# Kernel tuning notes

Hardware: AMD Instinct MI355X
Metric: run time of the kernel (lower is better)

The kernel has to match this reference:

```python
import jax, jax.numpy as jnp
import numpy as np

B, S, I, H = 256, 128, 1024, 512
SENT, DOC = 256, 512
SEGMENTS, MAX_POS = 4, 25
POS_SZ, SEG_SZ = 50, 50


def setup_inputs() -> dict:
    key = jax.random.key(0)
    ks = jax.random.split(key, 24)
    sc = 0.05
    rn = lambda k, shp: jax.random.normal(k, shp, jnp.float32) * sc
    pos_emb = rn(ks[20], (MAX_POS + 1, POS_SZ)).at[0].set(0.0)  # padding_idx=0
    seg_emb = rn(ks[22], (SEGMENTS + 1, SEG_SZ)).at[0].set(0.0)  # padding_idx=0
    return {
        "sentence_embeddings": jax.random.normal(ks[0], (B, S, I), jnp.float32),
        "num_sentences": jnp.full((B,), S, jnp.int32),
        "W_ih_f": rn(ks[1], (3 * H, I)), "W_hh_f": rn(ks[2], (3 * H, H)),
        "b_ih_f": jnp.zeros((3 * H,), jnp.float32), "b_hh_f": jnp.zeros((3 * H,), jnp.float32),
        "W_ih_b": rn(ks[3], (3 * H, I)), "W_hh_b": rn(ks[4], (3 * H, H)),
        "b_ih_b": jnp.zeros((3 * H,), jnp.float32), "b_hh_b": jnp.zeros((3 * H,), jnp.float32),
        "W_sent": rn(ks[5], (SENT, 2 * H)), "b_sent": jnp.zeros((SENT,), jnp.float32),
        "W_content": rn(ks[6], (1, SENT)), "b_content": jnp.zeros((1,), jnp.float32),
        "W_doc1": rn(ks[7], (DOC, SENT)), "b_doc1": jnp.zeros((DOC,), jnp.float32),
        "W_doc2": rn(ks[8], (SENT, DOC)), "b_doc2": jnp.zeros((SENT,), jnp.float32),
        "W_sim": rn(ks[9], (SENT, SENT)),
        "bias": jnp.zeros((1,), jnp.float32),
        "pos_emb": pos_emb, "W_pos": rn(ks[21], (1, POS_SZ)),
        "seg_emb": seg_emb, "W_seg": rn(ks[23], (1, SEG_SZ)),
    }


def _gru_dir(x_sbi, W_ih, W_hh, b_ih, b_hh):
    # x_sbi: [S,B,I] -> hidden states [S,B,H], PyTorch GRU gate order (r,z,n)
    h_dim = W_hh.shape[1]
    xp = jnp.einsum('sbi,gi->sbg', x_sbi, W_ih) + b_ih  # [S,B,3H]

    def step(h, xpt):
        gh = h @ W_hh.T + b_hh
        xr, xz, xn = jnp.split(xpt, 3, axis=-1)
        hr, hz, hn = jnp.split(gh, 3, axis=-1)
        r = jax.nn.sigmoid(xr + hr)
        z = jax.nn.sigmoid(xz + hz)
        n = jnp.tanh(xn + r * hn)
        h_new = (1.0 - z) * n + z * h
        return h_new, h_new

    h0 = jnp.zeros((x_sbi.shape[1], h_dim), x_sbi.dtype)
    _, hs = jax.lax.scan(step, h0, xp)
    return hs


def reference(sentence_embeddings, num_sentences, W_ih_f, W_hh_f, b_ih_f, b_hh_f,
              W_ih_b, W_hh_b, b_ih_b, b_hh_b, W_sent, b_sent, W_content, b_content,
              W_doc1, b_doc1, W_doc2, b_doc2, W_sim, bias, pos_emb, W_pos, seg_emb, W_seg):
    b, s, _ = sentence_embeddings.shape
    xt = jnp.swapaxes(sentence_embeddings, 0, 1)  # [S,B,I]
    fwd = _gru_dir(xt, W_ih_f, W_hh_f, b_ih_f, b_hh_f)
    bwd = _gru_dir(xt[::-1], W_ih_b, W_hh_b, b_ih_b, b_hh_b)[::-1]
    rnn_out = jnp.swapaxes(jnp.concatenate([fwd, bwd], -1), 0, 1)  # [B,S,2H]

    sent = jax.nn.relu(rnn_out @ W_sent.T + b_sent)              # [B,S,SENT]
    content = (sent @ W_content.T + b_content)[..., 0]            # [B,S]
    avg = sent.sum(1) / num_sentences[:, None].astype(sent.dtype) # [B,SENT]
    doc = jnp.tanh(avg @ W_doc1.T + b_doc1) @ W_doc2.T + b_doc2   # [B,SENT]
    salience = jnp.einsum('bsd,bd->bs', sent, doc)

    abs_pos = jnp.arange(1, s + 1)
    chunk = jnp.round(num_sentences.astype(jnp.float32) / SEGMENTS)[:, None]
    rel_pos = jnp.clip(jnp.ceil(abs_pos[None, :].astype(jnp.float32) / chunk), 0, SEGMENTS).astype(jnp.int32)
    abs_pos_c = jnp.clip(abs_pos, 0, MAX_POS)
    pos_logits = (pos_emb[abs_pos_c] @ W_pos.T)[..., 0][None, :]  # [1,S]
    seg_logits = (seg_emb[rel_pos] @ W_seg.T)[..., 0]             # [B,S]

    static = content + salience + pos_logits + seg_logits + bias  # [B,S]

    sent_t = jnp.swapaxes(sent, 0, 1)   # [S,B,SENT]
    static_t = static.T                  # [S,B]

    def step(summary, inp):
        s_t, st_t = inp
        nov = -jnp.einsum('bi,ij,bj->b', s_t, W_sim, jnp.tanh(summary))
        logit = st_t + nov
        summary = summary + s_t * jax.nn.sigmoid(logit)[:, None]
        return summary, logit

    _, logits_t = jax.lax.scan(step, jnp.zeros_like(sent_t[0]), (sent_t, static_t))
    return logits_t.T  # [B,S]
```

## Files before the change

kernel.cpp:

```cpp
#include <hip/hip_runtime.h>
#include <math.h>

#define B_    256
#define S_    128
#define I_    1024
#define H_    512
#define G3_   1536
#define SENT_ 256
#define DOC_  512
#define CH_   16

__device__ __forceinline__ float sigmoidf_(float x) { return 1.f / (1.f + expf(-x)); }

__global__ __launch_bounds__(256) void xp_gemm_kernel(
    const float* __restrict__ x,
    const float* __restrict__ Wf, const float* __restrict__ Wb,
    const float* __restrict__ bf, const float* __restrict__ bb,
    float* __restrict__ xq, int c0)
{
    const int nt   = blockIdx.x % 12;
    const int rest = blockIdx.x / 12;
    const int dir  = rest >> 5;
    const int mt   = rest & 31;
    const int m0   = mt * 128;
    const int n0   = nt * 128;
    const int tl   = m0 >> 8;
    const int b0x  = m0 & 255;
    const int s    = dir ? (S_ - 1 - (c0 + tl)) : (c0 + tl);
    const float* __restrict__ W    = dir ? Wb : Wf;
    const float* __restrict__ bias = dir ? bb : bf;
    float* __restrict__ outp = xq + (size_t)(dir * CH_ + tl) * B_ * G3_;

    __shared__ float Al[16][132];
    __shared__ float Bl[16][132];

    const int tid = threadIdx.x;
    const int tx = tid & 15, ty = tid >> 4;
    float acc[8][8] = {};

    for (int k0 = 0; k0 < I_; k0 += 16) {
        #pragma unroll
        for (int u = 0; u < 2; ++u) {
            const int fi = u * 256 + tid;
            const int r = fi >> 2, k4 = (fi & 3) * 4;
            const float4 v = *(const float4*)
                &x[((size_t)(b0x + r) * S_ + s) * (size_t)I_ + k0 + k4];
            Al[k4+0][r] = v.x; Al[k4+1][r] = v.y; Al[k4+2][r] = v.z; Al[k4+3][r] = v.w;
        }
        #pragma unroll
        for (int u = 0; u < 2; ++u) {
            const int fi = u * 256 + tid;
            const int c = fi >> 2, k4 = (fi & 3) * 4;
            const float4 v = *(const float4*)&W[(size_t)(n0 + c) * I_ + k0 + k4];
            Bl[k4+0][c] = v.x; Bl[k4+1][c] = v.y; Bl[k4+2][c] = v.z; Bl[k4+3][c] = v.w;
        }
        __syncthreads();
        #pragma unroll
        for (int k = 0; k < 16; ++k) {
            const float4 a0 = *(const float4*)&Al[k][ty * 4];
            const float4 a1 = *(const float4*)&Al[k][64 + ty * 4];
            const float4 b0 = *(const float4*)&Bl[k][tx * 4];
            const float4 b1 = *(const float4*)&Bl[k][64 + tx * 4];
            const float av[8] = {a0.x,a0.y,a0.z,a0.w,a1.x,a1.y,a1.z,a1.w};
            const float bv[8] = {b0.x,b0.y,b0.z,b0.w,b1.x,b1.y,b1.z,b1.w};
            #pragma unroll
            for (int i = 0; i < 8; ++i)
                #pragma unroll
                for (int jj = 0; jj < 8; ++jj)
                    acc[i][jj] += av[i] * bv[jj];
        }
        __syncthreads();
    }

    #pragma unroll
    for (int i = 0; i < 8; ++i) {
        const int rloc = (i < 4) ? (ty * 4 + i) : (64 + ty * 4 + (i - 4));
        const int b = b0x + rloc;
        #pragma unroll
        for (int cgv = 0; cgv < 2; ++cgv) {
            const int n = n0 + cgv * 64 + tx * 4;
            const float4 o = { acc[i][cgv*4+0] + bias[n+0],
                               acc[i][cgv*4+1] + bias[n+1],
                               acc[i][cgv*4+2] + bias[n+2],
                               acc[i][cgv*4+3] + bias[n+3] };
            *(float4*)&outp[(size_t)b * G3_ + n] = o;
        }
    }
}

__global__ __launch_bounds__(256) void sent_gemm_kernel(
    const float* __restrict__ A, const float* __restrict__ W,
    const float* __restrict__ bias, float* __restrict__ outp)
{
    const int nt = blockIdx.x & 1;
    const int mt = blockIdx.x >> 1;
    const int m0 = mt * 128, n0 = nt * 128;
    constexpr int K = 1024;

    __shared__ float Al[16][132];
    __shared__ float Bl[16][132];
    const int tid = threadIdx.x;
    const int tx = tid & 15, ty = tid >> 4;
    float acc[8][8] = {};

    for (int k0 = 0; k0 < K; k0 += 16) {
        #pragma unroll
        for (int u = 0; u < 2; ++u) {
            const int fi = u * 256 + tid;
            const int r = fi >> 2, k4 = (fi & 3) * 4;
            const float4 v = *(const float4*)&A[(size_t)(m0 + r) * K + k0 + k4];
            Al[k4+0][r] = v.x; Al[k4+1][r] = v.y; Al[k4+2][r] = v.z; Al[k4+3][r] = v.w;
        }
        #pragma unroll
        for (int u = 0; u < 2; ++u) {
            const int fi = u * 256 + tid;
            const int c = fi >> 2, k4 = (fi & 3) * 4;
            const float4 v = *(const float4*)&W[(size_t)(n0 + c) * K + k0 + k4];
            Bl[k4+0][c] = v.x; Bl[k4+1][c] = v.y; Bl[k4+2][c] = v.z; Bl[k4+3][c] = v.w;
        }
        __syncthreads();
        #pragma unroll
        for (int k = 0; k < 16; ++k) {
            const float4 a0 = *(const float4*)&Al[k][ty * 4];
            const float4 a1 = *(const float4*)&Al[k][64 + ty * 4];
            const float4 b0 = *(const float4*)&Bl[k][tx * 4];
            const float4 b1 = *(const float4*)&Bl[k][64 + tx * 4];
            const float av[8] = {a0.x,a0.y,a0.z,a0.w,a1.x,a1.y,a1.z,a1.w};
            const float bv[8] = {b0.x,b0.y,b0.z,b0.w,b1.x,b1.y,b1.z,b1.w};
            #pragma unroll
            for (int i = 0; i < 8; ++i)
                #pragma unroll
                for (int jj = 0; jj < 8; ++jj)
                    acc[i][jj] += av[i] * bv[jj];
        }
        __syncthreads();
    }

    #pragma unroll
    for (int i = 0; i < 8; ++i) {
        const int m = m0 + ((i < 4) ? (ty * 4 + i) : (64 + ty * 4 + (i - 4)));
        #pragma unroll
        for (int cgv = 0; cgv < 2; ++cgv) {
            const int n = n0 + cgv * 64 + tx * 4;
            const float4 o = { fmaxf(acc[i][cgv*4+0] + bias[n+0], 0.f),
                               fmaxf(acc[i][cgv*4+1] + bias[n+1], 0.f),
                               fmaxf(acc[i][cgv*4+2] + bias[n+2], 0.f),
                               fmaxf(acc[i][cgv*4+3] + bias[n+3], 0.f) };
            *(float4*)&outp[(size_t)m * SENT_ + n] = o;
        }
    }
}

__global__ __launch_bounds__(256) void gru_step_kernel(
    const float* __restrict__ xq,
    const float* __restrict__ Whf, const float* __restrict__ Whb,
    const float* __restrict__ bhf, const float* __restrict__ bhb,
    float* __restrict__ rnn, int t)
{
    __shared__ float hl[32][68];
    __shared__ float wl[3][32][66];

    const int bid = blockIdx.x;
    const int r8 = bid & 7;
    const int dir = (r8 < 4) ? 0 : 1;
    const int idx = (bid >> 3) * 4 + (r8 & 3);
    const int b0 = (idx >> 4) * 32;
    const int j0 = (idx & 15) * 32;
    const float* __restrict__ Wh = dir ? Whb : Whf;
    const float* __restrict__ bh = dir ? bhb : bhf;
    const int tid = threadIdx.x;
    const int tc = tid & 31, tr = tid >> 5;
    const int rr0 = tr * 4;
    const int j = j0 + tc;
    const int tl = t & (CH_ - 1);
    const int s  = dir ? (S_ - 1 - t) : t;
    const int sp = dir ? s + 1 : s - 1;
    const float bh0 = bh[j], bh1 = bh[512 + j], bh2 = bh[1024 + j];

    float acc[4][3] = {};
    if (t > 0) {
        for (int kb = 0; kb < 8; ++kb) {
            const int k0 = kb * 64;
            #pragma unroll
            for (int u = 0; u < 2; ++u) {
                const int f = u * 256 + tid;
                const int r = f >> 4, k4 = (f & 15) * 4;
                const float4 v = *(const float4*)
                    &rnn[((size_t)(b0 + r) * S_ + sp) * 1024 + dir * 512 + k0 + k4];
                *(float4*)&hl[r][k4] = v;
            }
            #pragma unroll
            for (int u = 0; u < 6; ++u) {
                const int f = u * 256 + tid;
                const int row = f >> 4, k4 = (f & 15) * 4;
                const int g = row >> 5, c = row & 31;
                const float4 v = *(const float4*)
                    &Wh[((size_t)(g * 512 + j0 + c)) * 512 + k0 + k4];
                wl[g][c][k4+0] = v.x; wl[g][c][k4+1] = v.y;
                wl[g][c][k4+2] = v.z; wl[g][c][k4+3] = v.w;
            }
            __syncthreads();
            #pragma unroll
            for (int k = 0; k < 64; k += 2) {
                const float2 h0 = *(const float2*)&hl[rr0+0][k];
                const float2 h1 = *(const float2*)&hl[rr0+1][k];
                const float2 h2 = *(const float2*)&hl[rr0+2][k];
                const float2 h3 = *(const float2*)&hl[rr0+3][k];
                #pragma unroll
                for (int g = 0; g < 3; ++g) {
                    const float2 w = *(const float2*)&wl[g][tc][k];
                    acc[0][g] += h0.x * w.x + h0.y * w.y;
                    acc[1][g] += h1.x * w.x + h1.y * w.y;
                    acc[2][g] += h2.x * w.x + h2.y * w.y;
                    acc[3][g] += h3.x * w.x + h3.y * w.y;
                }
            }
            __syncthreads();
        }
    }

    const float* __restrict__ xp = xq + (size_t)(dir * CH_ + tl) * B_ * G3_;
    #pragma unroll
    for (int i = 0; i < 4; ++i) {
        const int b = b0 + rr0 + i;
        const size_t xbase = (size_t)b * G3_ + j;
        const float xr = xp[xbase];
        const float xz = xp[xbase + 512];
        const float xn = xp[xbase + 1024];
        const float r_ = sigmoidf_(xr + acc[i][0] + bh0);
        const float z_ = sigmoidf_(xz + acc[i][1] + bh1);
        const float n_ = tanhf(xn + r_ * (acc[i][2] + bh2));
        const float hp = (t == 0) ? 0.f
            : rnn[((size_t)b * S_ + sp) * 1024 + dir * 512 + j];
        rnn[((size_t)b * S_ + s) * 1024 + dir * 512 + j] = (1.f - z_) * n_ + z_ * hp;
    }
}

__global__ __launch_bounds__(256) void avg_kernel(
    const float* __restrict__ sent, const int* __restrict__ ns, float* __restrict__ avg)
{
    const int b = blockIdx.x, jj = threadIdx.x;
    float a = 0.f;
    for (int s = 0; s < S_; ++s) a += sent[((size_t)b * S_ + s) * SENT_ + jj];
    avg[b * SENT_ + jj] = a / (float)ns[b];
}

__global__ __launch_bounds__(256) void doc_kernel(
    const float* __restrict__ avg,
    const float* __restrict__ W1, const float* __restrict__ b1,
    const float* __restrict__ W2, const float* __restrict__ b2,
    float* __restrict__ doc)
{
    const int b = blockIdx.x, tid = threadIdx.x;
    __shared__ float al[SENT_];
    __shared__ float t1[DOC_];
    al[tid] = avg[b * SENT_ + tid];
    __syncthreads();
    #pragma unroll
    for (int o = 0; o < 2; ++o) {
        const int row = o * 256 + tid;
        float acc = b1[row];
        for (int i = 0; i < SENT_; i += 4) {
            const float4 wv = *(const float4*)&W1[(size_t)row * SENT_ + i];
            acc += wv.x * al[i] + wv.y * al[i+1] + wv.z * al[i+2] + wv.w * al[i+3];
        }
        t1[row] = tanhf(acc);
    }
    __syncthreads();
    float acc = b2[tid];
    for (int i = 0; i < DOC_; i += 4) {
        const float4 wv = *(const float4*)&W2[(size_t)tid * DOC_ + i];
        acc += wv.x * t1[i] + wv.y * t1[i+1] + wv.z * t1[i+2] + wv.w * t1[i+3];
    }
    doc[b * SENT_ + tid] = acc;
}

__global__ __launch_bounds__(256) void static_kernel(
    const float* __restrict__ sent, const float* __restrict__ doc,
    const float* __restrict__ Wc, const float* __restrict__ bC,
    const float* __restrict__ pose, const float* __restrict__ Wpos,
    const float* __restrict__ sege, const float* __restrict__ Wseg,
    const float* __restrict__ biasp, const int* __restrict__ ns,
    float* __restrict__ statb)
{
    const int w = threadIdx.x >> 6, lane = threadIdx.x & 63;
    const int m = blockIdx.x * 4 + w;
    const int b = m >> 7, s = m & 127;
    const float4 se = *(const float4*)&sent[(size_t)m * SENT_ + lane * 4];
    const float4 wc = *(const float4*)&Wc[lane * 4];
    const float4 dc = *(const float4*)&doc[(size_t)b * SENT_ + lane * 4];
    float p = se.x * (wc.x + dc.x) + se.y * (wc.y + dc.y)
            + se.z * (wc.z + dc.z) + se.w * (wc.w + dc.w);
    if (lane < 50) {
        const int pidx = min(s + 1, 25);
        p += pose[pidx * 50 + lane] * Wpos[lane];
        const float chunk = rintf((float)ns[b] / 4.0f);
        float relf = ceilf((float)(s + 1) / chunk);
        relf = fminf(fmaxf(relf, 0.f), 4.f);
        const int rel = (int)relf;
        p += sege[rel * 50 + lane] * Wseg[lane];
    }
    #pragma unroll
    for (int o = 32; o > 0; o >>= 1) p += __shfl_down(p, o, 64);
    if (lane == 0) statb[m] = p + bC[0] + biasp[0];
}

__global__ __launch_bounds__(256) void scan_kernel(
    const float* __restrict__ sent, const float* __restrict__ statb,
    const float* __restrict__ Wsim, float* __restrict__ out)
{
    const int b = blockIdx.x;
    const int jj = threadIdx.x;
    __shared__ float summ[SENT_];
    __shared__ float sv[SENT_];
    __shared__ float red[4];
    summ[jj] = 0.f;
    __syncthreads();
    for (int t = 0; t < S_; ++t) {
        const float th = tanhf(summ[jj]);
        sv[jj] = sent[((size_t)b * S_ + t) * SENT_ + jj];
        __syncthreads();
        float a0 = 0.f, a1 = 0.f, a2 = 0.f, a3 = 0.f;
        #pragma unroll 4
        for (int i = 0; i < SENT_; i += 4) {
            a0 += sv[i+0] * Wsim[(i+0) * SENT_ + jj];
            a1 += sv[i+1] * Wsim[(i+1) * SENT_ + jj];
            a2 += sv[i+2] * Wsim[(i+2) * SENT_ + jj];
            a3 += sv[i+3] * Wsim[(i+3) * SENT_ + jj];
        }
        float m = (a0 + a1 + a2 + a3) * th;
        #pragma unroll
        for (int o = 32; o > 0; o >>= 1) m += __shfl_down(m, o, 64);
        if ((jj & 63) == 0) red[jj >> 6] = m;
        __syncthreads();
        const float nov = -(red[0] + red[1] + red[2] + red[3]);
        const float logit = statb[b * S_ + t] + nov;
        const float sig = sigmoidf_(logit);
        summ[jj] += sv[jj] * sig;
        if (jj == 0) out[b * S_ + t] = logit;
        __syncthreads();
    }
}

extern "C" void kernel_launch(void* const* d_in, const int* in_sizes, int n_in,
                              void* d_out, int out_size, void* d_ws, size_t ws_size,
                              hipStream_t stream)
{
    const float* x     = (const float*)d_in[0];
    const int*   ns    = (const int*)  d_in[1];
    const float* Wihf  = (const float*)d_in[2];
    const float* Whhf  = (const float*)d_in[3];
    const float* bihf  = (const float*)d_in[4];
    const float* bhhf  = (const float*)d_in[5];
    const float* Wihb  = (const float*)d_in[6];
    const float* Whhb  = (const float*)d_in[7];
    const float* bihb  = (const float*)d_in[8];
    const float* bhhb  = (const float*)d_in[9];
    const float* Wsent = (const float*)d_in[10];
    const float* bsent = (const float*)d_in[11];
    const float* Wcont = (const float*)d_in[12];
    const float* bcont = (const float*)d_in[13];
    const float* Wdoc1 = (const float*)d_in[14];
    const float* bdoc1 = (const float*)d_in[15];
    const float* Wdoc2 = (const float*)d_in[16];
    const float* bdoc2 = (const float*)d_in[17];
    const float* Wsim  = (const float*)d_in[18];
    const float* biasp = (const float*)d_in[19];
    const float* pose  = (const float*)d_in[20];
    const float* Wpos  = (const float*)d_in[21];
    const float* sege  = (const float*)d_in[22];
    const float* Wseg  = (const float*)d_in[23];
    float* out = (float*)d_out;

    float* ws      = (float*)d_ws;
    float* rnn     = ws;
    float* region0 = rnn + (size_t)B_ * S_ * (2 * H_);
    float* xq      = region0;
    float* sent    = region0;
    float* statb   = region0 + (size_t)2 * CH_ * B_ * G3_;
    float* avg     = statb + (size_t)B_ * S_;
    float* doc     = avg + (size_t)B_ * SENT_;

    for (int c = 0; c < S_ / CH_; ++c) {
        xp_gemm_kernel<<<dim3(768), dim3(256), 0, stream>>>(
            x, Wihf, Wihb, bihf, bihb, xq, c * CH_);
        for (int tl = 0; tl < CH_; ++tl) {
            gru_step_kernel<<<dim3(256), dim3(256), 0, stream>>>(
                xq, Whhf, Whhb, bhhf, bhhb, rnn, c * CH_ + tl);
        }
    }

    sent_gemm_kernel<<<dim3(512), dim3(256), 0, stream>>>(rnn, Wsent, bsent, sent);

    avg_kernel<<<dim3(256), dim3(256), 0, stream>>>(sent, ns, avg);
    doc_kernel<<<dim3(256), dim3(256), 0, stream>>>(avg, Wdoc1, bdoc1, Wdoc2, bdoc2, doc);
    static_kernel<<<dim3(8192), dim3(256), 0, stream>>>(
        sent, doc, Wcont, bcont, pose, Wpos, sege, Wseg, biasp, ns, statb);

    scan_kernel<<<dim3(256), dim3(256), 0, stream>>>(sent, statb, Wsim, out);
}
```

Baseline: 8.397 ms.

## Precompute sent@W_sim via GEMM for the scan and halve the GRU step tile

The novelty term s_t·W_sim·tanh(summary) is reassociated so P = sent·W_sim is computed once for all timesteps by a batched GEMM. The scan then becomes a single-wavefront dot product of P with tanh(summary), with no shared memory and no barriers per step. Separately, the GRU step kernel tile is cut from 32 to 16 hidden columns, doubling the grid to 512 blocks for more parallelism, at the cost of loading the h tile twice as often. P reuses the rnn workspace region, which is dead by the time the scan runs.

```diff
diff --git a/kernel.cpp b/kernel.cpp
--- a/kernel.cpp
+++ b/kernel.cpp
@@ -151,6 +151,67 @@
     }
 }
 
+__global__ __launch_bounds__(256) void p_gemm_kernel(
+    const float* __restrict__ A, const float* __restrict__ W,
+    float* __restrict__ outp)
+{
+    const int nt = blockIdx.x & 1;
+    const int mt = blockIdx.x >> 1;
+    const int m0 = mt * 128, n0 = nt * 128;
+    constexpr int K = 256;
+
+    __shared__ float Al[16][132];
+    __shared__ float Bl[16][132];
+    const int tid = threadIdx.x;
+    const int tx = tid & 15, ty = tid >> 4;
+    float acc[8][8] = {};
+
+    for (int k0 = 0; k0 < K; k0 += 16) {
+        #pragma unroll
+        for (int u = 0; u < 2; ++u) {
+            const int fi = u * 256 + tid;
+            const int r = fi >> 2, k4 = (fi & 3) * 4;
+            const float4 v = *(const float4*)&A[(size_t)(m0 + r) * K + k0 + k4];
+            Al[k4+0][r] = v.x; Al[k4+1][r] = v.y; Al[k4+2][r] = v.z; Al[k4+3][r] = v.w;
+        }
+        #pragma unroll
+        for (int u = 0; u < 2; ++u) {
+            const int fi = u * 256 + tid;
+            const int kr = fi >> 5, c4 = (fi & 31) * 4;
+            const float4 v = *(const float4*)&W[(size_t)(k0 + kr) * SENT_ + n0 + c4];
+            *(float4*)&Bl[kr][c4] = v;
+        }
+        __syncthreads();
+        #pragma unroll
+        for (int k = 0; k < 16; ++k) {
+            const float4 a0 = *(const float4*)&Al[k][ty * 4];
+            const float4 a1 = *(const float4*)&Al[k][64 + ty * 4];
+            const float4 b0 = *(const float4*)&Bl[k][tx * 4];
+            const float4 b1 = *(const float4*)&Bl[k][64 + tx * 4];
+            const float av[8] = {a0.x,a0.y,a0.z,a0.w,a1.x,a1.y,a1.z,a1.w};
+            const float bv[8] = {b0.x,b0.y,b0.z,b0.w,b1.x,b1.y,b1.z,b1.w};
+            #pragma unroll
+            for (int i = 0; i < 8; ++i)
+                #pragma unroll
+                for (int jj = 0; jj < 8; ++jj)
+                    acc[i][jj] += av[i] * bv[jj];
+        }
+        __syncthreads();
+    }
+
+    #pragma unroll
+    for (int i = 0; i < 8; ++i) {
+        const int m = m0 + ((i < 4) ? (ty * 4 + i) : (64 + ty * 4 + (i - 4)));
+        #pragma unroll
+        for (int cgv = 0; cgv < 2; ++cgv) {
+            const int n = n0 + cgv * 64 + tx * 4;
+            const float4 o = { acc[i][cgv*4+0], acc[i][cgv*4+1],
+                               acc[i][cgv*4+2], acc[i][cgv*4+3] };
+            *(float4*)&outp[(size_t)m * SENT_ + n] = o;
+        }
+    }
+}
+
 __global__ __launch_bounds__(256) void gru_step_kernel(
     const float* __restrict__ xq,
     const float* __restrict__ Whf, const float* __restrict__ Whb,
@@ -158,26 +219,26 @@
     float* __restrict__ rnn, int t)
 {
     __shared__ float hl[32][68];
-    __shared__ float wl[3][32][66];
+    __shared__ float wl[3][16][66];
 
     const int bid = blockIdx.x;
     const int r8 = bid & 7;
     const int dir = (r8 < 4) ? 0 : 1;
     const int idx = (bid >> 3) * 4 + (r8 & 3);
-    const int b0 = (idx >> 4) * 32;
-    const int j0 = (idx & 15) * 32;
+    const int b0 = (idx >> 5) * 32;
+    const int j0 = (idx & 31) * 16;
     const float* __restrict__ Wh = dir ? Whb : Whf;
     const float* __restrict__ bh = dir ? bhb : bhf;
     const int tid = threadIdx.x;
-    const int tc = tid & 31, tr = tid >> 5;
-    const int rr0 = tr * 4;
+    const int tc = tid & 15, tr = tid >> 4;
+    const int rr0 = tr * 2;
     const int j = j0 + tc;
     const int tl = t & (CH_ - 1);
     const int s  = dir ? (S_ - 1 - t) : t;
     const int sp = dir ? s + 1 : s - 1;
     const float bh0 = bh[j], bh1 = bh[512 + j], bh2 = bh[1024 + j];
 
-    float acc[4][3] = {};
+    float acc[2][3] = {};
     if (t > 0) {
         for (int kb = 0; kb < 8; ++kb) {
             const int k0 = kb * 64;
@@ -190,10 +251,10 @@
                 *(float4*)&hl[r][k4] = v;
             }
             #pragma unroll
-            for (int u = 0; u < 6; ++u) {
+            for (int u = 0; u < 3; ++u) {
                 const int f = u * 256 + tid;
                 const int row = f >> 4, k4 = (f & 15) * 4;
-                const int g = row >> 5, c = row & 31;
+                const int g = row >> 4, c = row & 15;
                 const float4 v = *(const float4*)
                     &Wh[((size_t)(g * 512 + j0 + c)) * 512 + k0 + k4];
                 wl[g][c][k4+0] = v.x; wl[g][c][k4+1] = v.y;
@@ -204,15 +265,11 @@
             for (int k = 0; k < 64; k += 2) {
                 const float2 h0 = *(const float2*)&hl[rr0+0][k];
                 const float2 h1 = *(const float2*)&hl[rr0+1][k];
-                const float2 h2 = *(const float2*)&hl[rr0+2][k];
-                const float2 h3 = *(const float2*)&hl[rr0+3][k];
                 #pragma unroll
                 for (int g = 0; g < 3; ++g) {
                     const float2 w = *(const float2*)&wl[g][tc][k];
                     acc[0][g] += h0.x * w.x + h0.y * w.y;
                     acc[1][g] += h1.x * w.x + h1.y * w.y;
-                    acc[2][g] += h2.x * w.x + h2.y * w.y;
-                    acc[3][g] += h3.x * w.x + h3.y * w.y;
                 }
             }
             __syncthreads();
@@ -221,7 +278,7 @@
 
     const float* __restrict__ xp = xq + (size_t)(dir * CH_ + tl) * B_ * G3_;
     #pragma unroll
-    for (int i = 0; i < 4; ++i) {
+    for (int i = 0; i < 2; ++i) {
         const int b = b0 + rr0 + i;
         const size_t xbase = (size_t)b * G3_ + j;
         const float xr = xp[xbase];
@@ -305,40 +362,26 @@
     if (lane == 0) statb[m] = p + bC[0] + biasp[0];
 }
 
-__global__ __launch_bounds__(256) void scan_kernel(
-    const float* __restrict__ sent, const float* __restrict__ statb,
-    const float* __restrict__ Wsim, float* __restrict__ out)
+__global__ __launch_bounds__(64) void scan2_kernel(
+    const float* __restrict__ sent, const float* __restrict__ P,
+    const float* __restrict__ statb, float* __restrict__ out)
 {
     const int b = blockIdx.x;
-    const int jj = threadIdx.x;
-    __shared__ float summ[SENT_];
-    __shared__ float sv[SENT_];
-    __shared__ float red[4];
-    summ[jj] = 0.f;
-    __syncthreads();
+    const int lane = threadIdx.x;
+    float4 summ = {0.f, 0.f, 0.f, 0.f};
     for (int t = 0; t < S_; ++t) {
-        const float th = tanhf(summ[jj]);
-        sv[jj] = sent[((size_t)b * S_ + t) * SENT_ + jj];
-        __syncthreads();
-        float a0 = 0.f, a1 = 0.f, a2 = 0.f, a3 = 0.f;
-        #pragma unroll 4
-        for (int i = 0; i < SENT_; i += 4) {
-            a0 += sv[i+0] * Wsim[(i+0) * SENT_ + jj];
-            a1 += sv[i+1] * Wsim[(i+1) * SENT_ + jj];
-            a2 += sv[i+2] * Wsim[(i+2) * SENT_ + jj];
-            a3 += sv[i+3] * Wsim[(i+3) * SENT_ + jj];
-        }
-        float m = (a0 + a1 + a2 + a3) * th;
-        #pragma unroll
-        for (int o = 32; o > 0; o >>= 1) m += __shfl_down(m, o, 64);
-        if ((jj & 63) == 0) red[jj >> 6] = m;
-        __syncthreads();
-        const float nov = -(red[0] + red[1] + red[2] + red[3]);
-        const float logit = statb[b * S_ + t] + nov;
+        const size_t row = ((size_t)b * S_ + t) * SENT_ + lane * 4;
+        const float4 pv = *(const float4*)&P[row];
+        const float4 sv = *(const float4*)&sent[row];
+        float m = pv.x * tanhf(summ.x) + pv.y * tanhf(summ.y)
+                + pv.z * tanhf(summ.z) + pv.w * tanhf(summ.w);
+        #pragma unroll
+        for (int o = 1; o < 64; o <<= 1) m += __shfl_xor(m, o, 64);
+        const float logit = statb[b * S_ + t] - m;
         const float sig = sigmoidf_(logit);
-        summ[jj] += sv[jj] * sig;
-        if (jj == 0) out[b * S_ + t] = logit;
-        __syncthreads();
+        summ.x += sv.x * sig; summ.y += sv.y * sig;
+        summ.z += sv.z * sig; summ.w += sv.w * sig;
+        if (lane == 0) out[b * S_ + t] = logit;
     }
 }
 
@@ -374,6 +417,7 @@
 
     float* ws      = (float*)d_ws;
     float* rnn     = ws;
+    float* P       = ws;
     float* region0 = rnn + (size_t)B_ * S_ * (2 * H_);
     float* xq      = region0;
     float* sent    = region0;
@@ -385,7 +429,7 @@
         xp_gemm_kernel<<<dim3(768), dim3(256), 0, stream>>>(
             x, Wihf, Wihb, bihf, bihb, xq, c * CH_);
         for (int tl = 0; tl < CH_; ++tl) {
-            gru_step_kernel<<<dim3(256), dim3(256), 0, stream>>>(
+            gru_step_kernel<<<dim3(512), dim3(256), 0, stream>>>(
                 xq, Whhf, Whhb, bhhf, bhhb, rnn, c * CH_ + tl);
         }
     }
@@ -397,5 +441,6 @@
     static_kernel<<<dim3(8192), dim3(256), 0, stream>>>(
         sent, doc, Wcont, bcont, pose, Wpos, sege, Wseg, biasp, ns, statb);
 
-    scan_kernel<<<dim3(256), dim3(256), 0, stream>>>(sent, statb, Wsim, out);
-}
+    p_gemm_kernel<<<dim3(512), dim3(256), 0, stream>>>(sent, Wsim, P);
+    scan2_kernel<<<dim3(256), dim3(64), 0, stream>>>(sent, P, statb, out);
+}
```

After: 7.605 ms. 9.4% less time.
